# Performance work log

Hardware: AMD Instinct MI355X
Metric: run time of the kernel (lower is better)

The kernel has to match this reference:

```python
import jax, jax.numpy as jnp
import numpy as np

N_NODES = 100000
N_EDGES = 1600000
N_FEATS = 128
HIDDEN = 20
N_GRAPHS = 256
N_CLASSES = 2


def setup_inputs() -> dict:
    key = jax.random.key(0)
    ks = jax.random.split(key, 12)
    x = jax.random.normal(ks[0], (N_NODES, N_FEATS), dtype=jnp.float32)
    edge_index = jax.random.randint(ks[1], (2, N_EDGES), 0, N_NODES, dtype=jnp.int64)
    batch = jnp.sort(jax.random.randint(ks[2], (N_NODES,), 0, N_GRAPHS, dtype=jnp.int64))
    def lin_init(k, fan_in, fan_out):
        kw, kb = jax.random.split(k)
        bound = 1.0 / np.sqrt(fan_in)
        W = jax.random.uniform(kw, (fan_in, fan_out), minval=-bound, maxval=bound, dtype=jnp.float32)
        b = jax.random.uniform(kb, (fan_out,), minval=-bound, maxval=bound, dtype=jnp.float32)
        return W, b
    W1, b1 = lin_init(ks[3], N_FEATS, HIDDEN)
    W2, b2 = lin_init(ks[4], HIDDEN, HIDDEN)
    W3, b3 = lin_init(ks[5], HIDDEN, HIDDEN)
    Wl, bl = lin_init(ks[6], 2 * HIDDEN, N_CLASSES)
    return {"x": x, "edge_index": edge_index, "batch": batch,
            "W1": W1, "b1": b1, "W2": W2, "b2": b2, "W3": W3, "b3": b3,
            "Wl": Wl, "bl": bl}


def gin_conv(x, src, dst, W, b):
    # GINConv with eps=0: mlp((1+eps)*x + sum_{j in N(i)} x_j)
    agg = jax.ops.segment_sum(x[src], dst, num_segments=x.shape[0])
    return (x + agg) @ W + b


def reference(x, edge_index, batch, W1, b1, W2, b2, W3, b3, Wl, bl):
    src, dst = edge_index[0], edge_index[1]
    h = jax.nn.relu(gin_conv(x, src, dst, W1, b1))
    h = jax.nn.relu(gin_conv(h, src, dst, W2, b2))
    h = jax.nn.relu(gin_conv(h, src, dst, W3, b3))  # [N, HIDDEN]
    # global max / mean pool per graph
    out1 = jax.ops.segment_max(h, batch, num_segments=N_GRAPHS)
    sums = jax.ops.segment_sum(h, batch, num_segments=N_GRAPHS)
    counts = jax.ops.segment_sum(jnp.ones((h.shape[0],), h.dtype), batch, num_segments=N_GRAPHS)
    out2 = sums / jnp.maximum(counts, 1.0)[:, None]
    pooled = jnp.concatenate([out1, out2], axis=-1)  # [G, 2*HIDDEN]
    return pooled @ Wl + bl
```

## Files before the change

### kernel.cpp

```cpp
#include <hip/hip_runtime.h>
#include <hip/hip_fp16.h>
#include <math.h>

#define N_NODES 100000
#define N_EDGES 1600000
#define N_FEATS 128
#define HIDDEN 20
#define N_GRAPHS 256

#define TILE 256
#define NB ((N_NODES + TILE - 1) / TILE)
#define SLOTS 5120
#define YSTRIDE 32

__device__ __half g_yh[2][(size_t)N_NODES * YSTRIDE];
__device__ float  g_facc[(size_t)N_NODES * HIDDEN];
__device__ int    g_part[(size_t)NB * SLOTS];
__device__ int    g_cursor[NB];
__device__ int    g_bbase[NB];
__device__ int    g_rowptr[N_NODES + 1];
__device__ int    g_col[N_EDGES];

__device__ __forceinline__ int detect_is64(const int* __restrict__ e32) {
    int acc = 0;
    #pragma unroll
    for (int j = 0; j < 8; j++) {
        int k = j * (N_EDGES / 8) + 997 * j + 13;
        acc |= e32[2 * k + 1];
    }
    return acc == 0;
}

__device__ __forceinline__ void load_edge(const void* eidx, int is64, int e,
                                          int& s, int& d) {
    if (is64) {
        const long long* e64 = (const long long*)eidx;
        s = (int)e64[e];
        d = (int)e64[N_EDGES + e];
    } else {
        const int* e32 = (const int*)eidx;
        s = e32[e];
        d = e32[N_EDGES + e];
    }
}

__global__ __launch_bounds__(512) void zero_kernel() {
    const int i = threadIdx.x;
    if (i < NB) g_cursor[i] = 0;
}

__global__ __launch_bounds__(512) void part_kernel(const void* __restrict__ eidx) {
    __shared__ int hist[NB];
    __shared__ int base[NB];
    const int t = threadIdx.x;
    const int e0 = blockIdx.x * 4096;
    for (int i = t; i < NB; i += 512) hist[i] = 0;
    const int is64 = detect_is64((const int*)eidx);
    __syncthreads();

    int sc[8], dc[8];
    #pragma unroll
    for (int k = 0; k < 8; k++) {
        const int e = e0 + k * 512 + t;
        sc[k] = -1; dc[k] = 0;
        if (e < N_EDGES) {
            int s, d;
            load_edge(eidx, is64, e, s, d);
            if ((unsigned)s < N_NODES && (unsigned)d < N_NODES) {
                sc[k] = s; dc[k] = d;
                atomicAdd(&hist[d >> 8], 1);
            }
        }
    }
    __syncthreads();
    for (int b = t; b < NB; b += 512) {
        const int c = hist[b];
        base[b] = c ? atomicAdd(&g_cursor[b], c) : 0;
        hist[b] = 0;
    }
    __syncthreads();
    #pragma unroll
    for (int k = 0; k < 8; k++) {
        if (sc[k] >= 0) {
            const int b = dc[k] >> 8;
            const int r = atomicAdd(&hist[b], 1);
            const int pos = base[b] + r;
            if (pos < SLOTS)
                g_part[(size_t)b * SLOTS + pos] = (sc[k] << 8) | (dc[k] & 255);
        }
    }
}

__global__ __launch_bounds__(512) void scanbase_kernel() {
    __shared__ int lds[512];
    const int t = threadIdx.x;
    int v = (t < NB) ? min(g_cursor[t], SLOTS) : 0;
    lds[t] = v;
    __syncthreads();
    for (int off = 1; off < 512; off <<= 1) {
        int u = (t >= off) ? lds[t - off] : 0;
        __syncthreads();
        lds[t] += u;
        __syncthreads();
    }
    if (t < NB) g_bbase[t] = lds[t] - v;
    if (t == 511) g_rowptr[N_NODES] = lds[511];
}

__global__ __launch_bounds__(512) void bucketsort_kernel() {
    __shared__ int hist[TILE];
    __shared__ int pfx[TILE];
    __shared__ int cur[TILE];
    __shared__ int sorted[SLOTS];
    const int t = threadIdx.x;
    const int b = blockIdx.x;
    const int cnt = min(g_cursor[b], SLOTS);
    const int base = g_bbase[b];
    if (t < TILE) hist[t] = 0;
    __syncthreads();
    const int* __restrict__ part = g_part + (size_t)b * SLOTS;
    for (int i = t; i < cnt; i += 512) atomicAdd(&hist[part[i] & 255], 1);
    __syncthreads();
    if (t < TILE) pfx[t] = hist[t];
    __syncthreads();
    for (int off = 1; off < TILE; off <<= 1) {
        int u = (t < TILE && t >= off) ? pfx[t - off] : 0;
        __syncthreads();
        if (t < TILE) pfx[t] += u;
        __syncthreads();
    }
    if (t < TILE) {
        const int ex = pfx[t] - hist[t];
        cur[t] = ex;
        const int node = b * TILE + t;
        if (node < N_NODES) g_rowptr[node] = base + ex;
    }
    __syncthreads();
    for (int i = t; i < cnt; i += 512) {
        const int rec = part[i];
        const int r = atomicAdd(&cur[rec & 255], 1);
        sorted[r] = rec >> 8;
    }
    __syncthreads();
    for (int i = t; i < cnt; i += 512) g_col[base + i] = sorted[i];
}

__global__ __launch_bounds__(256) void mm1_kernel(const float* __restrict__ x,
                                                  const float* __restrict__ W) {
    __shared__ float ldsWp[N_FEATS * HIDDEN];
    const int t = threadIdx.x;
    for (int i = t; i < N_FEATS * HIDDEN; i += 256) {
        const int korig = i / HIDDEN;
        const int c = i - korig * HIDDEN;
        const int jl = korig & 31;
        const int q = korig >> 5;
        ldsWp[(jl * 4 + q) * HIDDEN + c] = W[i];
    }
    __syncthreads();
    const int r = t >> 2;
    const int q = t & 3;
    const int row = blockIdx.x * 64 + r;
    const bool valid = row < N_NODES;

    float4 v[8];
    if (valid) {
        const float4* rp = (const float4*)&x[(size_t)row * N_FEATS + q * 32];
        #pragma unroll
        for (int i = 0; i < 8; i++) v[i] = rp[i];
    }
    float4 a0 = {0,0,0,0}, a1 = {0,0,0,0}, a2 = {0,0,0,0}, a3 = {0,0,0,0}, a4 = {0,0,0,0};
    if (valid) {
        #pragma unroll
        for (int i = 0; i < 8; i++) {
            const float xv[4] = {v[i].x, v[i].y, v[i].z, v[i].w};
            #pragma unroll
            for (int jj = 0; jj < 4; jj++) {
                const int jl = i * 4 + jj;
                const float4* wp = (const float4*)&ldsWp[(jl * 4 + q) * HIDDEN];
                const float xs = xv[jj];
                float4 w0 = wp[0], w1 = wp[1], w2 = wp[2], w3 = wp[3], w4 = wp[4];
                a0.x = fmaf(xs, w0.x, a0.x); a0.y = fmaf(xs, w0.y, a0.y);
                a0.z = fmaf(xs, w0.z, a0.z); a0.w = fmaf(xs, w0.w, a0.w);
                a1.x = fmaf(xs, w1.x, a1.x); a1.y = fmaf(xs, w1.y, a1.y);
                a1.z = fmaf(xs, w1.z, a1.z); a1.w = fmaf(xs, w1.w, a1.w);
                a2.x = fmaf(xs, w2.x, a2.x); a2.y = fmaf(xs, w2.y, a2.y);
                a2.z = fmaf(xs, w2.z, a2.z); a2.w = fmaf(xs, w2.w, a2.w);
                a3.x = fmaf(xs, w3.x, a3.x); a3.y = fmaf(xs, w3.y, a3.y);
                a3.z = fmaf(xs, w3.z, a3.z); a3.w = fmaf(xs, w3.w, a3.w);
                a4.x = fmaf(xs, w4.x, a4.x); a4.y = fmaf(xs, w4.y, a4.y);
                a4.z = fmaf(xs, w4.z, a4.z); a4.w = fmaf(xs, w4.w, a4.w);
            }
        }
    }
    float acc[20] = {a0.x, a0.y, a0.z, a0.w, a1.x, a1.y, a1.z, a1.w,
                     a2.x, a2.y, a2.z, a2.w, a3.x, a3.y, a3.z, a3.w,
                     a4.x, a4.y, a4.z, a4.w};
    #pragma unroll
    for (int off = 1; off <= 2; off <<= 1) {
        #pragma unroll
        for (int c = 0; c < 20; c++) acc[c] += __shfl_xor(acc[c], off);
    }
    if (valid) {
        __half* yp = &g_yh[0][(size_t)row * YSTRIDE];
        if (q == 0) {
            __half2 h0 = __float22half2_rn(make_float2(acc[0], acc[1]));
            __half2 h1 = __float22half2_rn(make_float2(acc[2], acc[3]));
            __half2 h2 = __float22half2_rn(make_float2(acc[4], acc[5]));
            __half2 h3 = __float22half2_rn(make_float2(acc[6], acc[7]));
            uint4 u; u.x = *(unsigned*)&h0; u.y = *(unsigned*)&h1;
            u.z = *(unsigned*)&h2; u.w = *(unsigned*)&h3;
            *(uint4*)&yp[0] = u;
        } else if (q == 1) {
            __half2 h0 = __float22half2_rn(make_float2(acc[8], acc[9]));
            __half2 h1 = __float22half2_rn(make_float2(acc[10], acc[11]));
            __half2 h2 = __float22half2_rn(make_float2(acc[12], acc[13]));
            __half2 h3 = __float22half2_rn(make_float2(acc[14], acc[15]));
            uint4 u; u.x = *(unsigned*)&h0; u.y = *(unsigned*)&h1;
            u.z = *(unsigned*)&h2; u.w = *(unsigned*)&h3;
            *(uint4*)&yp[8] = u;
        } else if (q == 2) {
            __half2 h0 = __float22half2_rn(make_float2(acc[16], acc[17]));
            __half2 h1 = __float22half2_rn(make_float2(acc[18], acc[19]));
            uint2 u; u.x = *(unsigned*)&h0; u.y = *(unsigned*)&h1;
            *(uint2*)&yp[16] = u;
        }
    }
}

template<bool FINAL>
__global__ __launch_bounds__(320) void gt_kernel(const float* __restrict__ bias,
                                                 const float* __restrict__ W,
                                                 int src) {
    const __half* __restrict__ y = g_yh[src];
    __shared__ float hrow[64][HIDDEN + 1];
    __shared__ float ldsW[HIDDEN * HIDDEN];
    __shared__ float ldsB[HIDDEN];
    const int t = threadIdx.x;
    if (!FINAL) {
        for (int i = t; i < HIDDEN * HIDDEN; i += 320) ldsW[i] = W[i];
        if (t < HIDDEN) ldsB[t] = bias[t];
    }
    const int nl = t / 5;
    const int chunk = t - nl * 5;
    const int node = blockIdx.x * 64 + nl;
    float sx = 0.f, sy = 0.f, sz = 0.f, sw = 0.f;
    if (node < N_NODES) {
        const int beg = g_rowptr[node];
        const int end = g_rowptr[node + 1];
        const int cb = chunk * 4;
        int i = beg;
        for (; i + 8 <= end; i += 8) {
            int s[8];
            #pragma unroll
            for (int k = 0; k < 8; k++) s[k] = g_col[i + k];
            uint2 u[8];
            #pragma unroll
            for (int k = 0; k < 8; k++)
                u[k] = *(const uint2*)&y[(size_t)s[k] * YSTRIDE + cb];
            #pragma unroll
            for (int k = 0; k < 8; k++) {
                const float2 a = __half22float2(*(const __half2*)&u[k].x);
                const float2 b = __half22float2(*(const __half2*)&u[k].y);
                sx += a.x; sy += a.y; sz += b.x; sw += b.y;
            }
        }
        for (; i + 4 <= end; i += 4) {
            const int s0 = g_col[i + 0];
            const int s1 = g_col[i + 1];
            const int s2 = g_col[i + 2];
            const int s3 = g_col[i + 3];
            const uint2 u0 = *(const uint2*)&y[(size_t)s0 * YSTRIDE + cb];
            const uint2 u1 = *(const uint2*)&y[(size_t)s1 * YSTRIDE + cb];
            const uint2 u2 = *(const uint2*)&y[(size_t)s2 * YSTRIDE + cb];
            const uint2 u3 = *(const uint2*)&y[(size_t)s3 * YSTRIDE + cb];
            float2 a, b;
            a = __half22float2(*(const __half2*)&u0.x); b = __half22float2(*(const __half2*)&u0.y);
            sx += a.x; sy += a.y; sz += b.x; sw += b.y;
            a = __half22float2(*(const __half2*)&u1.x); b = __half22float2(*(const __half2*)&u1.y);
            sx += a.x; sy += a.y; sz += b.x; sw += b.y;
            a = __half22float2(*(const __half2*)&u2.x); b = __half22float2(*(const __half2*)&u2.y);
            sx += a.x; sy += a.y; sz += b.x; sw += b.y;
            a = __half22float2(*(const __half2*)&u3.x); b = __half22float2(*(const __half2*)&u3.y);
            sx += a.x; sy += a.y; sz += b.x; sw += b.y;
        }
        for (; i < end; i++) {
            const int s = g_col[i];
            const uint2 u = *(const uint2*)&y[(size_t)s * YSTRIDE + cb];
            const float2 f0 = __half22float2(*(const __half2*)&u.x);
            const float2 f1 = __half22float2(*(const __half2*)&u.y);
            sx += f0.x; sy += f0.y; sz += f1.x; sw += f1.y;
        }
        const uint2 u = *(const uint2*)&y[(size_t)node * YSTRIDE + cb];
        const float2 f0 = __half22float2(*(const __half2*)&u.x);
        const float2 f1 = __half22float2(*(const __half2*)&u.y);
        sx += f0.x; sy += f0.y; sz += f1.x; sw += f1.y;
    }
    if (FINAL) {
        if (node < N_NODES) {
            float4 o; o.x = sx; o.y = sy; o.z = sz; o.w = sw;
            *(float4*)&g_facc[(size_t)node * HIDDEN + chunk * 4] = o;
        }
        return;
    }
    if (node < N_NODES) {
        hrow[nl][chunk * 4 + 0] = sx;
        hrow[nl][chunk * 4 + 1] = sy;
        hrow[nl][chunk * 4 + 2] = sz;
        hrow[nl][chunk * 4 + 3] = sw;
    }
    __syncthreads();
    if (node < N_NODES) {
        float h[HIDDEN];
        #pragma unroll
        for (int c = 0; c < HIDDEN; c++) {
            float v = hrow[nl][c] + ldsB[c];
            h[c] = v > 0.f ? v : 0.f;
        }
        const int cb = chunk * 4;
        float s0 = 0.f, s1 = 0.f, s2 = 0.f, s3 = 0.f;
        #pragma unroll
        for (int k = 0; k < HIDDEN; k++) {
            const float* w = &ldsW[k * HIDDEN + cb];
            s0 = fmaf(h[k], w[0], s0);
            s1 = fmaf(h[k], w[1], s1);
            s2 = fmaf(h[k], w[2], s2);
            s3 = fmaf(h[k], w[3], s3);
        }
        __half2 o0 = __float22half2_rn(make_float2(s0, s1));
        __half2 o1 = __float22half2_rn(make_float2(s2, s3));
        uint2 u;
        u.x = *(unsigned*)&o0;
        u.y = *(unsigned*)&o1;
        *(uint2*)&g_yh[src ^ 1][(size_t)node * YSTRIDE + cb] = u;
    }
}

__global__ __launch_bounds__(256) void pool_kernel(const float* __restrict__ b3,
                                                   const void* __restrict__ batch,
                                                   const void* __restrict__ eidx,
                                                   const float* __restrict__ Wl,
                                                   const float* __restrict__ bl,
                                                   float* __restrict__ out) {
    const float* __restrict__ acc3 = g_facc;
    const int g = blockIdx.x;
    const int t = threadIdx.x;
    const int is64 = detect_is64((const int*)eidx);
    const int* b32 = (const int*)batch;
    const long long* b64 = (const long long*)batch;
    #define BAT(i) (is64 ? (int)b64[i] : b32[i])
    int lo = 0, hi = N_NODES;
    while (lo < hi) { int mid = (lo + hi) >> 1; if (BAT(mid) < g) lo = mid + 1; else hi = mid; }
    const int start = lo;
    lo = start; hi = N_NODES;
    while (lo < hi) { int mid = (lo + hi) >> 1; if (BAT(mid) < g + 1) lo = mid + 1; else hi = mid; }
    const int end = lo;
    #undef BAT

    float b3r[HIDDEN];
    #pragma unroll
    for (int c = 0; c < HIDDEN; c++) b3r[c] = b3[c];
    float mx[HIDDEN], sm[HIDDEN];
    #pragma unroll
    for (int c = 0; c < HIDDEN; c++) { mx[c] = 0.f; sm[c] = 0.f; }

    for (int i = start + t; i < end; i += 256) {
        const float4* rp = (const float4*)&acc3[(size_t)i * HIDDEN];
        float4 q[5] = {rp[0], rp[1], rp[2], rp[3], rp[4]};
        const float* r = (const float*)q;
        #pragma unroll
        for (int c = 0; c < HIDDEN; c++) {
            float v = r[c] + b3r[c];
            v = v > 0.f ? v : 0.f;
            mx[c] = fmaxf(mx[c], v);
            sm[c] += v;
        }
    }
    #pragma unroll
    for (int off = 32; off >= 1; off >>= 1) {
        #pragma unroll
        for (int c = 0; c < HIDDEN; c++) {
            mx[c] = fmaxf(mx[c], __shfl_xor(mx[c], off));
            sm[c] += __shfl_xor(sm[c], off);
        }
    }
    __shared__ float smx[4][HIDDEN];
    __shared__ float ssm[4][HIDDEN];
    const int wave = t >> 6, lane = t & 63;
    if (lane == 0) {
        #pragma unroll
        for (int c = 0; c < HIDDEN; c++) { smx[wave][c] = mx[c]; ssm[wave][c] = sm[c]; }
    }
    __syncthreads();
    if (t == 0) {
        float cnt = (float)(end - start);
        float pooled[2 * HIDDEN];
        #pragma unroll
        for (int c = 0; c < HIDDEN; c++) {
            float m = smx[0][c], s = ssm[0][c];
            #pragma unroll
            for (int w = 1; w < 4; w++) { m = fmaxf(m, smx[w][c]); s += ssm[w][c]; }
            pooled[c] = m;
            pooled[HIDDEN + c] = s / fmaxf(cnt, 1.f);
        }
        #pragma unroll
        for (int c = 0; c < 2; c++) {
            float o = bl[c];
            #pragma unroll
            for (int k = 0; k < 2 * HIDDEN; k++) o = fmaf(pooled[k], Wl[k * 2 + c], o);
            out[g * 2 + c] = o;
        }
    }
}

extern "C" void kernel_launch(void* const* d_in, const int* in_sizes, int n_in,
                              void* d_out, int out_size, void* d_ws, size_t ws_size,
                              hipStream_t stream) {
    const float* x    = (const float*)d_in[0];
    const void* eidx  = d_in[1];
    const void* batch = d_in[2];
    const float* W1  = (const float*)d_in[3];
    const float* b1  = (const float*)d_in[4];
    const float* W2  = (const float*)d_in[5];
    const float* b2  = (const float*)d_in[6];
    const float* W3  = (const float*)d_in[7];
    const float* b3  = (const float*)d_in[8];
    const float* Wl  = (const float*)d_in[9];
    const float* bl  = (const float*)d_in[10];
    float* out = (float*)d_out;
    (void)d_ws; (void)ws_size;

    const int mm1_blocks = (N_NODES + 63) / 64;
    const int gt_blocks  = (N_NODES + 63) / 64;

    zero_kernel<<<1, 512, 0, stream>>>();
    part_kernel<<<NB, 512, 0, stream>>>(eidx);
    scanbase_kernel<<<1, 512, 0, stream>>>();
    bucketsort_kernel<<<NB, 512, 0, stream>>>();

    mm1_kernel<<<mm1_blocks, 256, 0, stream>>>(x, W1);
    gt_kernel<false><<<gt_blocks, 320, 0, stream>>>(b1, W2, 0);
    gt_kernel<false><<<gt_blocks, 320, 0, stream>>>(b2, W3, 1);
    gt_kernel<true><<<gt_blocks, 320, 0, stream>>>(nullptr, nullptr, 0);
    pool_kernel<<<N_GRAPHS, 256, 0, stream>>>(b3, batch, eidx, Wl, bl, out);
}
```

Baseline: 147.4 us.

## Drop global scan kernel by using padded per-bucket CSR with begin/end arrays

Removes the single-block scanbase kernel by giving each bucket a fixed SLOTS-sized region in the column array and storing separate row-begin and row-end arrays instead of a compact rowptr. The bucket sort kernel is also widened to 1024 threads per block. This saves one kernel launch and a serial dependency, at the cost of a sparser column layout, an extra row-end load in the gather kernels, and higher per-block register pressure.

Measured after the change: 163.0 us. 1.11x slower.

```diff
diff --git a/kernel.cpp b/kernel.cpp
--- a/kernel.cpp
+++ b/kernel.cpp
@@ -17,9 +17,9 @@
 __device__ float  g_facc[(size_t)N_NODES * HIDDEN];
 __device__ int    g_part[(size_t)NB * SLOTS];
 __device__ int    g_cursor[NB];
-__device__ int    g_bbase[NB];
-__device__ int    g_rowptr[N_NODES + 1];
-__device__ int    g_col[N_EDGES];
+__device__ int    g_rowbeg[NB * TILE];
+__device__ int    g_rowend[NB * TILE];
+__device__ int    g_col[(size_t)NB * SLOTS];
 
 __device__ __forceinline__ int detect_is64(const int* __restrict__ e32) {
     int acc = 0;
@@ -91,23 +91,7 @@
     }
 }
 
-__global__ __launch_bounds__(512) void scanbase_kernel() {
-    __shared__ int lds[512];
-    const int t = threadIdx.x;
-    int v = (t < NB) ? min(g_cursor[t], SLOTS) : 0;
-    lds[t] = v;
-    __syncthreads();
-    for (int off = 1; off < 512; off <<= 1) {
-        int u = (t >= off) ? lds[t - off] : 0;
-        __syncthreads();
-        lds[t] += u;
-        __syncthreads();
-    }
-    if (t < NB) g_bbase[t] = lds[t] - v;
-    if (t == 511) g_rowptr[N_NODES] = lds[511];
-}
-
-__global__ __launch_bounds__(512) void bucketsort_kernel() {
+__global__ __launch_bounds__(1024) void bucketsort_kernel() {
     __shared__ int hist[TILE];
     __shared__ int pfx[TILE];
     __shared__ int cur[TILE];
@@ -115,11 +99,11 @@
     const int t = threadIdx.x;
     const int b = blockIdx.x;
     const int cnt = min(g_cursor[b], SLOTS);
-    const int base = g_bbase[b];
+    const int base = b * SLOTS;
     if (t < TILE) hist[t] = 0;
     __syncthreads();
     const int* __restrict__ part = g_part + (size_t)b * SLOTS;
-    for (int i = t; i < cnt; i += 512) atomicAdd(&hist[part[i] & 255], 1);
+    for (int i = t; i < cnt; i += 1024) atomicAdd(&hist[part[i] & 255], 1);
     __syncthreads();
     if (t < TILE) pfx[t] = hist[t];
     __syncthreads();
@@ -133,16 +117,19 @@
         const int ex = pfx[t] - hist[t];
         cur[t] = ex;
         const int node = b * TILE + t;
-        if (node < N_NODES) g_rowptr[node] = base + ex;
-    }
-    __syncthreads();
-    for (int i = t; i < cnt; i += 512) {
+        if (node < N_NODES) {
+            g_rowbeg[node] = base + ex;
+            g_rowend[node] = base + ex + hist[t];
+        }
+    }
+    __syncthreads();
+    for (int i = t; i < cnt; i += 1024) {
         const int rec = part[i];
         const int r = atomicAdd(&cur[rec & 255], 1);
         sorted[r] = rec >> 8;
     }
     __syncthreads();
-    for (int i = t; i < cnt; i += 512) g_col[base + i] = sorted[i];
+    for (int i = t; i < cnt; i += 1024) g_col[base + i] = sorted[i];
 }
 
 __global__ __launch_bounds__(256) void mm1_kernel(const float* __restrict__ x,
@@ -245,8 +232,8 @@
     const int node = blockIdx.x * 64 + nl;
     float sx = 0.f, sy = 0.f, sz = 0.f, sw = 0.f;
     if (node < N_NODES) {
-        const int beg = g_rowptr[node];
-        const int end = g_rowptr[node + 1];
+        const int beg = g_rowbeg[node];
+        const int end = g_rowend[node];
         const int cb = chunk * 4;
         int i = beg;
         for (; i + 8 <= end; i += 8) {
@@ -434,8 +421,7 @@
 
     zero_kernel<<<1, 512, 0, stream>>>();
     part_kernel<<<NB, 512, 0, stream>>>(eidx);
-    scanbase_kernel<<<1, 512, 0, stream>>>();
-    bucketsort_kernel<<<NB, 512, 0, stream>>>();
+    bucketsort_kernel<<<NB, 1024, 0, stream>>>();
 
     mm1_kernel<<<mm1_blocks, 256, 0, stream>>>(x, W1);
     gt_kernel<false><<<gt_blocks, 320, 0, stream>>>(b1, W2, 0);
```
